# Optimization experiments

Measured on AMD Instinct MI355X. Metric: run time of the kernel, lower is better.

Reference implementation:

```python
import jax, jax.numpy as jnp
import numpy as np

D_MODEL = 1024
NUM_HEADS = 16
HEAD_SIZE = D_MODEL // NUM_HEADS


def setup_inputs() -> dict:
    key = jax.random.key(0)
    ks = jax.random.split(key, 11)
    B, S, D = 4, 2048, D_MODEL
    scale = 1.0 / np.sqrt(D)
    inp = {
        "queries": jax.random.normal(ks[0], (B, S, D), jnp.float32),
        "keys": jax.random.normal(ks[1], (B, S, D), jnp.float32),
        "values": jax.random.normal(ks[2], (B, S, D), jnp.float32),
        "W_Q": jax.random.normal(ks[3], (D, D), jnp.float32) * scale,
        "b_Q": jax.random.normal(ks[4], (D,), jnp.float32) * 0.01,
        "W_K": jax.random.normal(ks[5], (D, D), jnp.float32) * scale,
        "b_K": jax.random.normal(ks[6], (D,), jnp.float32) * 0.01,
        "W_V": jax.random.normal(ks[7], (D, D), jnp.float32) * scale,
        "b_V": jax.random.normal(ks[8], (D,), jnp.float32) * 0.01,
        "W_O": jax.random.normal(ks[9], (D, D), jnp.float32) * scale,
        "b_O": jax.random.normal(ks[10], (D,), jnp.float32) * 0.01,
    }
    return inp


def _split_heads(x):
    B, S, D = x.shape
    return x.reshape(B, S, NUM_HEADS, HEAD_SIZE).transpose(0, 2, 1, 3)  # (B,H,S,hd)


def reference(queries, keys, values, W_Q, b_Q, W_K, b_K, W_V, b_V, W_O, b_O):
    # Linear projections (torch Linear: x @ W^T + b; here W stored as (D,D) used directly)
    q = _split_heads(queries @ W_Q + b_Q)  # (B,H,S,hd)
    k = _split_heads(keys @ W_K + b_K)
    v = _split_heads(values @ W_V + b_V)

    S = q.shape[2]
    scores = jnp.einsum("bhqd,bhkd->bhqk", q, k) / jnp.sqrt(jnp.float32(HEAD_SIZE))
    causal = jnp.tril(jnp.ones((S, S), dtype=bool))  # True where attention allowed
    scores = jnp.where(causal, scores, -jnp.inf)
    attn = jax.nn.softmax(scores, axis=-1)  # (B,H,S,S)

    ctx = jnp.einsum("bhqk,bhkd->bhqd", attn, v)  # (B,H,S,hd)
    B = ctx.shape[0]
    ctx = ctx.transpose(0, 2, 1, 3).reshape(B, S, D_MODEL)  # merge heads
    out = ctx @ W_O + b_O
    return out, jax.lax.stop_gradient(attn)
```

## Files before the change

kernel.cpp:

```cpp
#include <hip/hip_runtime.h>
#include <math.h>

#define D_MODEL 1024
#define NUM_HEADS 16
#define HEAD_SIZE 64
#define SEQ 2048
#define BATCH 4
#define M_PROJ (BATCH * SEQ)

__global__ __launch_bounds__(256) void gemm_bias_kernel(
    const float* __restrict__ A, const float* __restrict__ W,
    const float* __restrict__ bias, float* __restrict__ C,
    int M, int N, int K) {
  __shared__ float As[16][132];
  __shared__ float Ws[16][132];
  const int tid = threadIdx.x;
  const int bm = blockIdx.y * 128;
  const int bn = blockIdx.x * 128;
  const int tx = tid & 15;
  const int ty = tid >> 4;

  const int ar = tid >> 2;
  const int ac = (tid & 3) << 2;
  const int wk = tid >> 4;
  const int wc = (tid & 15) << 2;

  float acc[2][2][4][4] = {};

  for (int k0 = 0; k0 < K; k0 += 16) {
#pragma unroll
    for (int h = 0; h < 2; ++h) {
      const int r = ar + h * 64;
      float4 a4 =
          *reinterpret_cast<const float4*>(&A[(size_t)(bm + r) * K + k0 + ac]);
      As[ac + 0][r] = a4.x;
      As[ac + 1][r] = a4.y;
      As[ac + 2][r] = a4.z;
      As[ac + 3][r] = a4.w;
      float4 w4 = *reinterpret_cast<const float4*>(
          &W[(size_t)(k0 + wk) * N + bn + wc + h * 64]);
      *reinterpret_cast<float4*>(&Ws[wk][wc + h * 64]) = w4;
    }
    __syncthreads();
#pragma unroll
    for (int kk = 0; kk < 16; ++kk) {
      float4 a0 = *reinterpret_cast<const float4*>(&As[kk][ty << 2]);
      float4 a1 = *reinterpret_cast<const float4*>(&As[kk][64 + (ty << 2)]);
      float4 w0 = *reinterpret_cast<const float4*>(&Ws[kk][tx << 2]);
      float4 w1 = *reinterpret_cast<const float4*>(&Ws[kk][64 + (tx << 2)]);
      const float am[2][4] = {{a0.x, a0.y, a0.z, a0.w},
                              {a1.x, a1.y, a1.z, a1.w}};
      const float wn[2][4] = {{w0.x, w0.y, w0.z, w0.w},
                              {w1.x, w1.y, w1.z, w1.w}};
#pragma unroll
      for (int p = 0; p < 2; ++p)
#pragma unroll
        for (int q = 0; q < 2; ++q)
#pragma unroll
          for (int i = 0; i < 4; ++i)
#pragma unroll
            for (int j = 0; j < 4; ++j)
              acc[p][q][i][j] += am[p][i] * wn[q][j];
    }
    __syncthreads();
  }

  float4 bv[2];
  bv[0] = *reinterpret_cast<const float4*>(&bias[bn + (tx << 2)]);
  bv[1] = *reinterpret_cast<const float4*>(&bias[bn + 64 + (tx << 2)]);
#pragma unroll
  for (int p = 0; p < 2; ++p)
#pragma unroll
    for (int i = 0; i < 4; ++i) {
      const size_t row = (size_t)(bm + p * 64 + (ty << 2) + i);
#pragma unroll
      for (int q = 0; q < 2; ++q) {
        const float bb[4] = {bv[q].x, bv[q].y, bv[q].z, bv[q].w};
        float4 o;
        o.x = acc[p][q][i][0] + bb[0];
        o.y = acc[p][q][i][1] + bb[1];
        o.z = acc[p][q][i][2] + bb[2];
        o.w = acc[p][q][i][3] + bb[3];
        *reinterpret_cast<float4*>(
            &C[row * N + bn + q * 64 + (tx << 2)]) = o;
      }
    }
}

__global__ __launch_bounds__(256) void scores_kernel(
    const float* __restrict__ Q, const float* __restrict__ Kp,
    float* __restrict__ attn) {
  const int bh = blockIdx.y;
  const int b = bh >> 4;
  const int h = bh & 15;
  const int t = blockIdx.x;
  int qt = (int)((sqrtf(8.f * (float)t + 1.f) - 1.f) * 0.5f);
  while ((qt * (qt + 1)) / 2 > t) --qt;
  while (((qt + 1) * (qt + 2)) / 2 <= t) ++qt;
  const int kt = t - (qt * (qt + 1)) / 2;

  __shared__ float Qs[64][132];
  __shared__ float Ks[64][132];
  const int tid = threadIdx.x;
  const int tx = tid & 15;
  const int ty = tid >> 4;

  const int r = tid >> 1;
  const int cbase = (tid & 1) << 5;
  const float* qg = Q + ((size_t)(b * SEQ + qt * 128 + r)) * D_MODEL + h * 64;
  const float* kg = Kp + ((size_t)(b * SEQ + kt * 128 + r)) * D_MODEL + h * 64;
#pragma unroll
  for (int u = 0; u < 8; ++u) {
    const int c = cbase + (u << 2);
    float4 q4 = *reinterpret_cast<const float4*>(qg + c);
    Qs[c + 0][r] = q4.x; Qs[c + 1][r] = q4.y;
    Qs[c + 2][r] = q4.z; Qs[c + 3][r] = q4.w;
    float4 k4 = *reinterpret_cast<const float4*>(kg + c);
    Ks[c + 0][r] = k4.x; Ks[c + 1][r] = k4.y;
    Ks[c + 2][r] = k4.z; Ks[c + 3][r] = k4.w;
  }
  __syncthreads();

  float acc[2][2][4][4] = {};
#pragma unroll 8
  for (int d = 0; d < 64; ++d) {
    float4 q0 = *reinterpret_cast<const float4*>(&Qs[d][ty << 2]);
    float4 q1 = *reinterpret_cast<const float4*>(&Qs[d][64 + (ty << 2)]);
    float4 k0 = *reinterpret_cast<const float4*>(&Ks[d][tx << 2]);
    float4 k1 = *reinterpret_cast<const float4*>(&Ks[d][64 + (tx << 2)]);
    const float qm[2][4] = {{q0.x, q0.y, q0.z, q0.w},
                            {q1.x, q1.y, q1.z, q1.w}};
    const float kn[2][4] = {{k0.x, k0.y, k0.z, k0.w},
                            {k1.x, k1.y, k1.z, k1.w}};
#pragma unroll
    for (int p = 0; p < 2; ++p)
#pragma unroll
      for (int q = 0; q < 2; ++q)
#pragma unroll
        for (int i = 0; i < 4; ++i)
#pragma unroll
          for (int j = 0; j < 4; ++j)
            acc[p][q][i][j] += qm[p][i] * kn[q][j];
  }

#pragma unroll
  for (int p = 0; p < 2; ++p)
#pragma unroll
    for (int i = 0; i < 4; ++i) {
      const size_t row =
          (size_t)bh * SEQ + qt * 128 + p * 64 + (ty << 2) + i;
#pragma unroll
      for (int q = 0; q < 2; ++q) {
        float4 o;
        o.x = acc[p][q][i][0] * 0.125f;
        o.y = acc[p][q][i][1] * 0.125f;
        o.z = acc[p][q][i][2] * 0.125f;
        o.w = acc[p][q][i][3] * 0.125f;
        *reinterpret_cast<float4*>(
            &attn[row * SEQ + kt * 128 + q * 64 + (tx << 2)]) = o;
      }
    }
}

__global__ __launch_bounds__(256) void softmax_kernel(float* __restrict__ attn) {
  const size_t row = blockIdx.x;
  const int q = (int)(row & (SEQ - 1));
  const int n = q + 1;
  float* p = attn + row * (size_t)SEQ;
  const int tid = threadIdx.x;

  float v[8];
#pragma unroll
  for (int u = 0; u < 8; ++u) {
    const int i = tid + (u << 8);
    v[u] = (i < n) ? p[i] : -INFINITY;
  }
  float m = v[0];
#pragma unroll
  for (int u = 1; u < 8; ++u) m = fmaxf(m, v[u]);
#pragma unroll
  for (int off = 1; off < 64; off <<= 1) m = fmaxf(m, __shfl_xor(m, off, 64));
  __shared__ float redm[4];
  if ((tid & 63) == 0) redm[tid >> 6] = m;
  __syncthreads();
  m = fmaxf(fmaxf(redm[0], redm[1]), fmaxf(redm[2], redm[3]));

  float s = 0.f;
#pragma unroll
  for (int u = 0; u < 8; ++u) {
    const float e = expf(v[u] - m);
    v[u] = e;
    s += e;
  }
#pragma unroll
  for (int off = 1; off < 64; off <<= 1) s += __shfl_xor(s, off, 64);
  __shared__ float reds[4];
  if ((tid & 63) == 0) reds[tid >> 6] = s;
  __syncthreads();
  s = reds[0] + reds[1] + reds[2] + reds[3];

  const float inv = 1.f / s;
#pragma unroll
  for (int u = 0; u < 8; ++u) p[tid + (u << 8)] = v[u] * inv;
}

__global__ __launch_bounds__(256) void pv_kernel(
    const float* __restrict__ attn, const float* __restrict__ V,
    float* __restrict__ ctx) {
  const int qt = blockIdx.x;
  const int bh = blockIdx.y;
  const int b = bh >> 4;
  const int h = bh & 15;
  __shared__ float Ps[16][132];
  __shared__ float Vs[16][68];
  const int tid = threadIdx.x;
  const int tx = tid & 15;
  const int ty = tid >> 4;
  float acc[2][4][4] = {};

  const int kmax = (qt + 1) * 128;
  const float* arow = attn + ((size_t)bh * SEQ + qt * 128) * SEQ;
  const int pr = tid >> 2, pc = (tid & 3) << 2;
  const int vr = tid >> 4, vc = (tid & 15) << 2;

  for (int k0 = 0; k0 < kmax; k0 += 16) {
#pragma unroll
    for (int hh = 0; hh < 2; ++hh) {
      const int r = pr + hh * 64;
      float4 p4 =
          *reinterpret_cast<const float4*>(&arow[(size_t)r * SEQ + k0 + pc]);
      Ps[pc + 0][r] = p4.x; Ps[pc + 1][r] = p4.y;
      Ps[pc + 2][r] = p4.z; Ps[pc + 3][r] = p4.w;
    }
    float4 v4 = *reinterpret_cast<const float4*>(
        &V[(size_t)(b * SEQ + k0 + vr) * D_MODEL + h * 64 + vc]);
    *reinterpret_cast<float4*>(&Vs[vr][vc]) = v4;
    __syncthreads();
#pragma unroll
    for (int kk = 0; kk < 16; ++kk) {
      float4 a0 = *reinterpret_cast<const float4*>(&Ps[kk][ty << 2]);
      float4 a1 = *reinterpret_cast<const float4*>(&Ps[kk][64 + (ty << 2)]);
      float4 vv = *reinterpret_cast<const float4*>(&Vs[kk][tx << 2]);
      const float am[2][4] = {{a0.x, a0.y, a0.z, a0.w},
                              {a1.x, a1.y, a1.z, a1.w}};
      const float vn[4] = {vv.x, vv.y, vv.z, vv.w};
#pragma unroll
      for (int p = 0; p < 2; ++p)
#pragma unroll
        for (int i = 0; i < 4; ++i)
#pragma unroll
          for (int j = 0; j < 4; ++j)
            acc[p][i][j] += am[p][i] * vn[j];
    }
    __syncthreads();
  }

#pragma unroll
  for (int p = 0; p < 2; ++p)
#pragma unroll
    for (int i = 0; i < 4; ++i) {
      float4 o = {acc[p][i][0], acc[p][i][1], acc[p][i][2], acc[p][i][3]};
      *reinterpret_cast<float4*>(
          &ctx[(size_t)(b * SEQ + qt * 128 + p * 64 + (ty << 2) + i) *
                   D_MODEL +
               h * 64 + (tx << 2)]) = o;
    }
}

extern "C" void kernel_launch(void* const* d_in, const int* in_sizes, int n_in,
                              void* d_out, int out_size, void* d_ws,
                              size_t ws_size, hipStream_t stream) {
  const float* queries = (const float*)d_in[0];
  const float* keys = (const float*)d_in[1];
  const float* values = (const float*)d_in[2];
  const float* W_Q = (const float*)d_in[3];
  const float* b_Q = (const float*)d_in[4];
  const float* W_K = (const float*)d_in[5];
  const float* b_K = (const float*)d_in[6];
  const float* W_V = (const float*)d_in[7];
  const float* b_V = (const float*)d_in[8];
  const float* W_O = (const float*)d_in[9];
  const float* b_O = (const float*)d_in[10];

  float* out = (float*)d_out;
  float* attn = out + (size_t)BATCH * SEQ * D_MODEL;

  const size_t proj_elems = (size_t)M_PROJ * D_MODEL;
  float* Q = (float*)d_ws;
  float* K = Q + proj_elems;
  float* V = K + proj_elems;
  float* ctx = V + proj_elems;

  const dim3 blk(256);
  const dim3 gproj(D_MODEL / 128, M_PROJ / 128);

  gemm_bias_kernel<<<gproj, blk, 0, stream>>>(queries, W_Q, b_Q, Q, M_PROJ,
                                              D_MODEL, D_MODEL);
  gemm_bias_kernel<<<gproj, blk, 0, stream>>>(keys, W_K, b_K, K, M_PROJ,
                                              D_MODEL, D_MODEL);
  gemm_bias_kernel<<<gproj, blk, 0, stream>>>(values, W_V, b_V, V, M_PROJ,
                                              D_MODEL, D_MODEL);

  const int ntri = (SEQ / 128) * (SEQ / 128 + 1) / 2;
  scores_kernel<<<dim3(ntri, BATCH * NUM_HEADS), blk, 0, stream>>>(Q, K, attn);

  softmax_kernel<<<dim3(BATCH * NUM_HEADS * SEQ), blk, 0, stream>>>(attn);

  pv_kernel<<<dim3(SEQ / 128, BATCH * NUM_HEADS), blk, 0, stream>>>(attn, V,
                                                                    ctx);

  gemm_bias_kernel<<<gproj, blk, 0, stream>>>(ctx, W_O, b_O, out, M_PROJ,
                                              D_MODEL, D_MODEL);
}
```

Before: 2.687 ms.

## Use split-bf16 MFMA for projection GEMMs and attention score computation

Replaces the FP32 SIMT GEMMs for the Q/K/V/O projections and the QK^T score kernel with MFMA bf16 kernels. Each operand is split into hi and lo bf16 parts, and three products are accumulated to approximate FP32 accuracy. Operands are staged into LDS through global_load_lds, and the GEMM grid uses a swizzled block order. Extra split and transpose kernels, plus bf16 workspace buffers, add memory traffic and launches in exchange for matrix-core throughput, at some precision risk.

```diff
diff --git a/kernel.cpp b/kernel.cpp
--- a/kernel.cpp
+++ b/kernel.cpp
@@ -1,4 +1,5 @@
 #include <hip/hip_runtime.h>
+#include <hip/hip_bf16.h>
 #include <math.h>
 
 #define D_MODEL 1024
@@ -8,88 +9,162 @@
 #define BATCH 4
 #define M_PROJ (BATCH * SEQ)
 
-__global__ __launch_bounds__(256) void gemm_bias_kernel(
-    const float* __restrict__ A, const float* __restrict__ W,
+typedef __attribute__((ext_vector_type(8))) short bf16x8;
+typedef __attribute__((ext_vector_type(4))) float f32x4;
+
+__device__ inline float bf2f(ushort u) {
+  return __uint_as_float(((unsigned int)u) << 16);
+}
+__device__ inline ushort f2bf(float x) {
+  unsigned int b = __float_as_uint(x);
+  b += 0x7fffu + ((b >> 16) & 1u);
+  return (ushort)(b >> 16);
+}
+
+__device__ inline void gload_lds16(const void* g, void* l) {
+  __builtin_amdgcn_global_load_lds(
+      (const __attribute__((address_space(1))) void*)g,
+      (__attribute__((address_space(3))) void*)l, 16, 0, 0);
+}
+
+__global__ __launch_bounds__(256) void split_kernel(
+    const float* __restrict__ in, ushort* __restrict__ hi,
+    ushort* __restrict__ lo, int n4) {
+  for (int i = blockIdx.x * 256 + threadIdx.x; i < n4; i += gridDim.x * 256) {
+    float4 v = reinterpret_cast<const float4*>(in)[i];
+    const float xs[4] = {v.x, v.y, v.z, v.w};
+    ushort hh[4], ll[4];
+#pragma unroll
+    for (int j = 0; j < 4; ++j) {
+      hh[j] = f2bf(xs[j]);
+      ll[j] = f2bf(xs[j] - bf2f(hh[j]));
+    }
+    ushort4 h4, l4;
+    h4.x = hh[0]; h4.y = hh[1]; h4.z = hh[2]; h4.w = hh[3];
+    l4.x = ll[0]; l4.y = ll[1]; l4.z = ll[2]; l4.w = ll[3];
+    reinterpret_cast<ushort4*>(hi)[i] = h4;
+    reinterpret_cast<ushort4*>(lo)[i] = l4;
+  }
+}
+
+__global__ __launch_bounds__(256) void transpose_split_kernel(
+    const float* __restrict__ W, ushort* __restrict__ tHi,
+    ushort* __restrict__ tLo) {
+  __shared__ float tile[64][65];
+  const int kt = blockIdx.y << 6, nt = blockIdx.x << 6;
+  const int tx = threadIdx.x & 15, ty = threadIdx.x >> 4;
+#pragma unroll
+  for (int u = 0; u < 4; ++u) {
+    const int r = ty + (u << 4);
+    float4 v = *reinterpret_cast<const float4*>(
+        &W[(size_t)(kt + r) * D_MODEL + nt + (tx << 2)]);
+    tile[r][(tx << 2) + 0] = v.x;
+    tile[r][(tx << 2) + 1] = v.y;
+    tile[r][(tx << 2) + 2] = v.z;
+    tile[r][(tx << 2) + 3] = v.w;
+  }
+  __syncthreads();
+#pragma unroll
+  for (int u = 0; u < 4; ++u) {
+    const int n = ty + (u << 4);
+    ushort h[4], l[4];
+#pragma unroll
+    for (int i = 0; i < 4; ++i) {
+      const float x = tile[(tx << 2) + i][n];
+      h[i] = f2bf(x);
+      l[i] = f2bf(x - bf2f(h[i]));
+    }
+    ushort4 h4, l4;
+    h4.x = h[0]; h4.y = h[1]; h4.z = h[2]; h4.w = h[3];
+    l4.x = l[0]; l4.y = l[1]; l4.z = l[2]; l4.w = l[3];
+    *reinterpret_cast<ushort4*>(
+        &tHi[(size_t)(nt + n) * D_MODEL + kt + (tx << 2)]) = h4;
+    *reinterpret_cast<ushort4*>(
+        &tLo[(size_t)(nt + n) * D_MODEL + kt + (tx << 2)]) = l4;
+  }
+}
+
+__global__ __launch_bounds__(256) void mfma_gemm_kernel(
+    const ushort* __restrict__ Ahi, const ushort* __restrict__ Alo,
+    const ushort* __restrict__ Bhi, const ushort* __restrict__ Blo,
     const float* __restrict__ bias, float* __restrict__ C,
     int M, int N, int K) {
-  __shared__ float As[16][132];
-  __shared__ float Ws[16][132];
+  __shared__ short lds[16384];
   const int tid = threadIdx.x;
-  const int bm = blockIdx.y * 128;
-  const int bn = blockIdx.x * 128;
-  const int tx = tid & 15;
-  const int ty = tid >> 4;
-
-  const int ar = tid >> 2;
-  const int ac = (tid & 3) << 2;
-  const int wk = tid >> 4;
-  const int wc = (tid & 15) << 2;
-
-  float acc[2][2][4][4] = {};
-
-  for (int k0 = 0; k0 < K; k0 += 16) {
-#pragma unroll
-    for (int h = 0; h < 2; ++h) {
-      const int r = ar + h * 64;
-      float4 a4 =
-          *reinterpret_cast<const float4*>(&A[(size_t)(bm + r) * K + k0 + ac]);
-      As[ac + 0][r] = a4.x;
-      As[ac + 1][r] = a4.y;
-      As[ac + 2][r] = a4.z;
-      As[ac + 3][r] = a4.w;
-      float4 w4 = *reinterpret_cast<const float4*>(
-          &W[(size_t)(k0 + wk) * N + bn + wc + h * 64]);
-      *reinterpret_cast<float4*>(&Ws[wk][wc + h * 64]) = w4;
+  const int wid = tid >> 6, lane = tid & 63;
+
+  const int nbn = N >> 7;
+  const int cpx = gridDim.x >> 3;
+  const int swz = (blockIdx.x & 7) * cpx + (blockIdx.x >> 3);
+  const int bm = (swz / nbn) << 7;
+  const int bn = (swz % nbn) << 7;
+
+  const int rowoff = lane & 15;
+  const int koff = (lane >> 4) << 3;
+  const int wr = wid >> 1, wc = wid & 1;
+
+  f32x4 acc[4][4] = {};
+
+  for (int k0 = 0; k0 < K; k0 += 32) {
+#pragma unroll
+    for (int iss = 0; iss < 2; ++iss) {
+      const int f = (iss << 2) + wid;
+      const size_t arow = (size_t)(bm + f * 16 + rowoff) * K + k0 + koff;
+      const size_t brow = (size_t)(bn + f * 16 + rowoff) * K + k0 + koff;
+      gload_lds16(Ahi + arow, &lds[0 * 4096 + f * 512]);
+      gload_lds16(Alo + arow, &lds[1 * 4096 + f * 512]);
+      gload_lds16(Bhi + brow, &lds[2 * 4096 + f * 512]);
+      gload_lds16(Blo + brow, &lds[3 * 4096 + f * 512]);
     }
     __syncthreads();
-#pragma unroll
-    for (int kk = 0; kk < 16; ++kk) {
-      float4 a0 = *reinterpret_cast<const float4*>(&As[kk][ty << 2]);
-      float4 a1 = *reinterpret_cast<const float4*>(&As[kk][64 + (ty << 2)]);
-      float4 w0 = *reinterpret_cast<const float4*>(&Ws[kk][tx << 2]);
-      float4 w1 = *reinterpret_cast<const float4*>(&Ws[kk][64 + (tx << 2)]);
-      const float am[2][4] = {{a0.x, a0.y, a0.z, a0.w},
-                              {a1.x, a1.y, a1.z, a1.w}};
-      const float wn[2][4] = {{w0.x, w0.y, w0.z, w0.w},
-                              {w1.x, w1.y, w1.z, w1.w}};
-#pragma unroll
-      for (int p = 0; p < 2; ++p)
-#pragma unroll
-        for (int q = 0; q < 2; ++q)
-#pragma unroll
-          for (int i = 0; i < 4; ++i)
-#pragma unroll
-            for (int j = 0; j < 4; ++j)
-              acc[p][q][i][j] += am[p][i] * wn[q][j];
-    }
+
+    bf16x8 ah[4], al[4], bh[4], bl[4];
+#pragma unroll
+    for (int i = 0; i < 4; ++i) {
+      const int fa = wr * 4 + i;
+      const int fb = wc * 4 + i;
+      ah[i] = *reinterpret_cast<const bf16x8*>(&lds[0 * 4096 + fa * 512 + lane * 8]);
+      al[i] = *reinterpret_cast<const bf16x8*>(&lds[1 * 4096 + fa * 512 + lane * 8]);
+      bh[i] = *reinterpret_cast<const bf16x8*>(&lds[2 * 4096 + fb * 512 + lane * 8]);
+      bl[i] = *reinterpret_cast<const bf16x8*>(&lds[3 * 4096 + fb * 512 + lane * 8]);
+    }
+#pragma unroll
+    for (int mi = 0; mi < 4; ++mi)
+#pragma unroll
+      for (int ni = 0; ni < 4; ++ni) {
+        acc[mi][ni] = __builtin_amdgcn_mfma_f32_16x16x32_bf16(
+            ah[mi], bh[ni], acc[mi][ni], 0, 0, 0);
+        acc[mi][ni] = __builtin_amdgcn_mfma_f32_16x16x32_bf16(
+            ah[mi], bl[ni], acc[mi][ni], 0, 0, 0);
+        acc[mi][ni] = __builtin_amdgcn_mfma_f32_16x16x32_bf16(
+            al[mi], bh[ni], acc[mi][ni], 0, 0, 0);
+      }
     __syncthreads();
   }
 
-  float4 bv[2];
-  bv[0] = *reinterpret_cast<const float4*>(&bias[bn + (tx << 2)]);
-  bv[1] = *reinterpret_cast<const float4*>(&bias[bn + 64 + (tx << 2)]);
-#pragma unroll
-  for (int p = 0; p < 2; ++p)
-#pragma unroll
-    for (int i = 0; i < 4; ++i) {
-      const size_t row = (size_t)(bm + p * 64 + (ty << 2) + i);
-#pragma unroll
-      for (int q = 0; q < 2; ++q) {
-        const float bb[4] = {bv[q].x, bv[q].y, bv[q].z, bv[q].w};
-        float4 o;
-        o.x = acc[p][q][i][0] + bb[0];
-        o.y = acc[p][q][i][1] + bb[1];
-        o.z = acc[p][q][i][2] + bb[2];
-        o.w = acc[p][q][i][3] + bb[3];
-        *reinterpret_cast<float4*>(
-            &C[row * N + bn + q * 64 + (tx << 2)]) = o;
-      }
-    }
-}
-
-__global__ __launch_bounds__(256) void scores_kernel(
-    const float* __restrict__ Q, const float* __restrict__ Kp,
+  const int crowbase = bm + wr * 64 + ((lane >> 4) << 2);
+  const int ccolbase = bn + wc * 64 + (lane & 15);
+#pragma unroll
+  for (int ni = 0; ni < 4; ++ni) {
+    const int col = ccolbase + ni * 16;
+    const float bv = bias[col];
+#pragma unroll
+    for (int mi = 0; mi < 4; ++mi) {
+      const int row = crowbase + mi * 16;
+#pragma unroll
+      for (int j = 0; j < 4; ++j)
+        C[(size_t)(row + j) * N + col] = acc[mi][ni][j] + bv;
+    }
+  }
+}
+
+__global__ __launch_bounds__(256) void scores_mfma_kernel(
+    const ushort* __restrict__ Qhi, const ushort* __restrict__ Qlo,
+    const ushort* __restrict__ Khi, const ushort* __restrict__ Klo,
     float* __restrict__ attn) {
+  __shared__ short lds[32768];
+  const int tid = threadIdx.x;
+  const int wid = tid >> 6, lane = tid & 63;
   const int bh = blockIdx.y;
   const int b = bh >> 4;
   const int h = bh & 15;
@@ -99,67 +174,67 @@
   while (((qt + 1) * (qt + 2)) / 2 <= t) ++qt;
   const int kt = t - (qt * (qt + 1)) / 2;
 
-  __shared__ float Qs[64][132];
-  __shared__ float Ks[64][132];
-  const int tid = threadIdx.x;
-  const int tx = tid & 15;
-  const int ty = tid >> 4;
-
-  const int r = tid >> 1;
-  const int cbase = (tid & 1) << 5;
-  const float* qg = Q + ((size_t)(b * SEQ + qt * 128 + r)) * D_MODEL + h * 64;
-  const float* kg = Kp + ((size_t)(b * SEQ + kt * 128 + r)) * D_MODEL + h * 64;
-#pragma unroll
-  for (int u = 0; u < 8; ++u) {
-    const int c = cbase + (u << 2);
-    float4 q4 = *reinterpret_cast<const float4*>(qg + c);
-    Qs[c + 0][r] = q4.x; Qs[c + 1][r] = q4.y;
-    Qs[c + 2][r] = q4.z; Qs[c + 3][r] = q4.w;
-    float4 k4 = *reinterpret_cast<const float4*>(kg + c);
-    Ks[c + 0][r] = k4.x; Ks[c + 1][r] = k4.y;
-    Ks[c + 2][r] = k4.z; Ks[c + 3][r] = k4.w;
+  const int rowoff = lane & 15;
+  const int koff = (lane >> 4) << 3;
+  const int wr = wid >> 1, wc = wid & 1;
+
+  const size_t qbase = (size_t)(b * SEQ + qt * 128) * D_MODEL + h * 64;
+  const size_t kbase = (size_t)(b * SEQ + kt * 128) * D_MODEL + h * 64;
+#pragma unroll
+  for (int iss = 0; iss < 2; ++iss) {
+    const int f = (iss << 2) + wid;
+#pragma unroll
+    for (int s = 0; s < 2; ++s) {
+      const size_t qa = qbase + (size_t)(f * 16 + rowoff) * D_MODEL + s * 32 + koff;
+      const size_t ka = kbase + (size_t)(f * 16 + rowoff) * D_MODEL + s * 32 + koff;
+      const int lo_ = (f * 2 + s) * 512;
+      gload_lds16(Qhi + qa, &lds[0 * 8192 + lo_]);
+      gload_lds16(Qlo + qa, &lds[1 * 8192 + lo_]);
+      gload_lds16(Khi + ka, &lds[2 * 8192 + lo_]);
+      gload_lds16(Klo + ka, &lds[3 * 8192 + lo_]);
+    }
   }
   __syncthreads();
 
-  float acc[2][2][4][4] = {};
-#pragma unroll 8
-  for (int d = 0; d < 64; ++d) {
-    float4 q0 = *reinterpret_cast<const float4*>(&Qs[d][ty << 2]);
-    float4 q1 = *reinterpret_cast<const float4*>(&Qs[d][64 + (ty << 2)]);
-    float4 k0 = *reinterpret_cast<const float4*>(&Ks[d][tx << 2]);
-    float4 k1 = *reinterpret_cast<const float4*>(&Ks[d][64 + (tx << 2)]);
-    const float qm[2][4] = {{q0.x, q0.y, q0.z, q0.w},
-                            {q1.x, q1.y, q1.z, q1.w}};
-    const float kn[2][4] = {{k0.x, k0.y, k0.z, k0.w},
-                            {k1.x, k1.y, k1.z, k1.w}};
-#pragma unroll
-    for (int p = 0; p < 2; ++p)
-#pragma unroll
-      for (int q = 0; q < 2; ++q)
-#pragma unroll
-        for (int i = 0; i < 4; ++i)
-#pragma unroll
-          for (int j = 0; j < 4; ++j)
-            acc[p][q][i][j] += qm[p][i] * kn[q][j];
-  }
-
-#pragma unroll
-  for (int p = 0; p < 2; ++p)
+  f32x4 acc[4][4] = {};
+#pragma unroll
+  for (int s = 0; s < 2; ++s) {
+    bf16x8 ah[4], al[4], kh[4], kl[4];
 #pragma unroll
     for (int i = 0; i < 4; ++i) {
-      const size_t row =
-          (size_t)bh * SEQ + qt * 128 + p * 64 + (ty << 2) + i;
-#pragma unroll
-      for (int q = 0; q < 2; ++q) {
-        float4 o;
-        o.x = acc[p][q][i][0] * 0.125f;
-        o.y = acc[p][q][i][1] * 0.125f;
-        o.z = acc[p][q][i][2] * 0.125f;
-        o.w = acc[p][q][i][3] * 0.125f;
-        *reinterpret_cast<float4*>(
-            &attn[row * SEQ + kt * 128 + q * 64 + (tx << 2)]) = o;
+      const int fa = ((wr * 4 + i) * 2 + s) * 512 + lane * 8;
+      const int fb = ((wc * 4 + i) * 2 + s) * 512 + lane * 8;
+      ah[i] = *reinterpret_cast<const bf16x8*>(&lds[0 * 8192 + fa]);
+      al[i] = *reinterpret_cast<const bf16x8*>(&lds[1 * 8192 + fa]);
+      kh[i] = *reinterpret_cast<const bf16x8*>(&lds[2 * 8192 + fb]);
+      kl[i] = *reinterpret_cast<const bf16x8*>(&lds[3 * 8192 + fb]);
+    }
+#pragma unroll
+    for (int mi = 0; mi < 4; ++mi)
+#pragma unroll
+      for (int ni = 0; ni < 4; ++ni) {
+        acc[mi][ni] = __builtin_amdgcn_mfma_f32_16x16x32_bf16(
+            ah[mi], kh[ni], acc[mi][ni], 0, 0, 0);
+        acc[mi][ni] = __builtin_amdgcn_mfma_f32_16x16x32_bf16(
+            ah[mi], kl[ni], acc[mi][ni], 0, 0, 0);
+        acc[mi][ni] = __builtin_amdgcn_mfma_f32_16x16x32_bf16(
+            al[mi], kh[ni], acc[mi][ni], 0, 0, 0);
       }
-    }
+  }
+
+  const int crowbase = qt * 128 + wr * 64 + ((lane >> 4) << 2);
+  const int ccolbase = kt * 128 + wc * 64 + (lane & 15);
+#pragma unroll
+  for (int ni = 0; ni < 4; ++ni) {
+    const int col = ccolbase + ni * 16;
+#pragma unroll
+    for (int mi = 0; mi < 4; ++mi) {
+      const int row = crowbase + mi * 16;
+#pragma unroll
+      for (int j = 0; j < 4; ++j)
+        attn[((size_t)bh * SEQ + row + j) * SEQ + col] = acc[mi][ni][j] * 0.125f;
+    }
+  }
 }
 
 __global__ __launch_bounds__(256) void softmax_kernel(float* __restrict__ attn) {
@@ -262,8 +337,7 @@
       float4 o = {acc[p][i][0], acc[p][i][1], acc[p][i][2], acc[p][i][3]};
       *reinterpret_cast<float4*>(
           &ctx[(size_t)(b * SEQ + qt * 128 + p * 64 + (ty << 2) + i) *
-                   D_MODEL +
-               h * 64 + (tx << 2)]) = o;
+                   D_MODEL + h * 64 + (tx << 2)]) = o;
     }
 }
 
@@ -285,30 +359,46 @@
   float* out = (float*)d_out;
   float* attn = out + (size_t)BATCH * SEQ * D_MODEL;
 
-  const size_t proj_elems = (size_t)M_PROJ * D_MODEL;
+  const size_t PE = (size_t)M_PROJ * D_MODEL;
   float* Q = (float*)d_ws;
-  float* K = Q + proj_elems;
-  float* V = K + proj_elems;
-  float* ctx = V + proj_elems;
+  float* K = Q + PE;
+  float* V = K + PE;
+  float* ctx = V + PE;
+  ushort* Xhi = (ushort*)(ctx + PE);
+  ushort* Xlo = Xhi + PE;
+  ushort* Wthi = Xlo + PE;
+  ushort* Wtlo = Wthi + (size_t)D_MODEL * D_MODEL;
+  ushort* Qhi = Wtlo + (size_t)D_MODEL * D_MODEL;
+  ushort* Qlo = Qhi + PE;
+  ushort* Khi = Qlo + PE;
+  ushort* Klo = Khi + PE;
 
   const dim3 blk(256);
-  const dim3 gproj(D_MODEL / 128, M_PROJ / 128);
-
-  gemm_bias_kernel<<<gproj, blk, 0, stream>>>(queries, W_Q, b_Q, Q, M_PROJ,
-                                              D_MODEL, D_MODEL);
-  gemm_bias_kernel<<<gproj, blk, 0, stream>>>(keys, W_K, b_K, K, M_PROJ,
-                                              D_MODEL, D_MODEL);
-  gemm_bias_kernel<<<gproj, blk, 0, stream>>>(values, W_V, b_V, V, M_PROJ,
-                                              D_MODEL, D_MODEL);
+  const int n4 = (int)(PE / 4);
+
+  auto do_gemm = [&](const float* X, const float* W, const float* b,
+                     float* Cout) {
+    split_kernel<<<2048, blk, 0, stream>>>(X, Xhi, Xlo, n4);
+    transpose_split_kernel<<<dim3(16, 16), blk, 0, stream>>>(W, Wthi, Wtlo);
+    mfma_gemm_kernel<<<dim3(512), blk, 0, stream>>>(
+        Xhi, Xlo, Wthi, Wtlo, b, Cout, M_PROJ, D_MODEL, D_MODEL);
+  };
+
+  do_gemm(queries, W_Q, b_Q, Q);
+  do_gemm(keys, W_K, b_K, K);
+  do_gemm(values, W_V, b_V, V);
+
+  split_kernel<<<2048, blk, 0, stream>>>(Q, Qhi, Qlo, n4);
+  split_kernel<<<2048, blk, 0, stream>>>(K, Khi, Klo, n4);
 
   const int ntri = (SEQ / 128) * (SEQ / 128 + 1) / 2;
-  scores_kernel<<<dim3(ntri, BATCH * NUM_HEADS), blk, 0, stream>>>(Q, K, attn);
+  scores_mfma_kernel<<<dim3(ntri, BATCH * NUM_HEADS), blk, 0, stream>>>(
+      Qhi, Qlo, Khi, Klo, attn);
 
   softmax_kernel<<<dim3(BATCH * NUM_HEADS * SEQ), blk, 0, stream>>>(attn);
 
   pv_kernel<<<dim3(SEQ / 128, BATCH * NUM_HEADS), blk, 0, stream>>>(attn, V,
                                                                     ctx);
 
-  gemm_bias_kernel<<<gproj, blk, 0, stream>>>(ctx, W_O, b_O, out, M_PROJ,
-                                              D_MODEL, D_MODEL);
-}
+  do_gemm(ctx, W_O, b_O, out);
+}
```

Result: faster. 2.282 ms (-15.1%).
